# Performance work log

Hardware: AMD Instinct MI355X
Metric: run time of the kernel (lower is better)

## Reference

```python
import jax, jax.numpy as jnp
import numpy as np

B, T, H, CD, NC, S, D = 128, 256, 512, 128, 2048, 256, 9
EPS = 1e-5

def _lin(x, w, b):
    return x @ w.T + b

def _gru_cell(x, h, wih, whh, bih, bhh):
    gi = x @ wih.T + bih
    gh = h @ whh.T + bhh
    ir, iz, inn = jnp.split(gi, 3, axis=-1)
    hr, hz, hn = jnp.split(gh, 3, axis=-1)
    r = jax.nn.sigmoid(ir + hr)
    z = jax.nn.sigmoid(iz + hz)
    n = jnp.tanh(inn + r * hn)
    return (1.0 - z) * n + z * h

def _bn(x, g, b, m, v):
    # eval-mode BatchNorm1d over channel dim of [B,C,W]
    return (x - m[:, None]) * (g * jax.lax.rsqrt(v + EPS))[:, None] + b[:, None]

def _conv(x, w, b, stride, pad):
    y = jax.lax.conv_general_dilated(x, w, (stride,), [(pad, pad)], dimension_numbers=('NCW', 'OIW', 'NCW'))
    return y + b[:, None]

def _convT(x, w, b, stride, pad, out_pad):
    # torch ConvTranspose1d with weight [I,O,k] == dilated conv with flipped, transposed kernel
    k = w.shape[-1]
    w2 = jnp.flip(w, -1).transpose(1, 0, 2)  # [O,I,k]
    y = jax.lax.conv_general_dilated(x, w2, (1,), [(k - 1 - pad, k - 1 - pad + out_pad)], lhs_dilation=(stride,), dimension_numbers=('NCW', 'OIW', 'NCW'))
    return y + b[:, None]

def _gru_seq(x, h0, wih, whh, bih, bhh, reverse=False):
    def step(h, xt):
        hn = _gru_cell(xt, h, wih, whh, bih, bhh)
        return hn, hn
    _, ys = jax.lax.scan(step, h0, jnp.swapaxes(x, 0, 1), reverse=reverse)
    return jnp.swapaxes(ys, 0, 1)

def _forward(note, skel, skel_encoded, ehw, ehb, ifw, ifb, gfwih, gfwhh, gfbih, gfbhh, gbwih, gbwhh, gbbih, gbbhh, bn0g, bn0b, bn0m, bn0v, c1w, c1b, bn1g, bn1b, bn1m, bn1v, c2w, c2b, bn2g, bn2b, bn2m, bn2v, c3w, c3b, embed, ct1w, ct1b, dbn1g, dbn1b, dbn1m, dbn1v, ct2w, ct2b, dbn2g, dbn2b, dbn2m, dbn2v, dhw, dhb, g1wih, g1whh, g1bih, g1bhh, g2wih, g2whh, g2bih, g2bhh, nfw, nfb, samp_rand):
    sg = jax.lax.stop_gradient
    # ---- encoder ----
    hid = _lin(skel_encoded, ehw, ehb)                         # [B,H] shared init for both GRU dirs
    x = _lin(note, ifw, ifb)                                   # [B,T,H]
    fwd = _gru_seq(x, hid, gfwih, gfwhh, gfbih, gfbhh)
    bwd = _gru_seq(x, hid, gbwih, gbwhh, gbbih, gbbhh, reverse=True)
    out = jnp.concatenate([fwd, bwd], axis=-1).transpose(0, 2, 1)  # [B,2H,T]
    out = _bn(out, bn0g, bn0b, bn0m, bn0v)
    out = jax.nn.leaky_relu(_bn(_conv(out, c1w, c1b, 2, 1), bn1g, bn1b, bn1m, bn1v), 0.2)
    out = jax.nn.leaky_relu(_bn(_conv(out, c2w, c2b, 2, 1), bn2g, bn2b, bn2m, bn2v), 0.2)
    z = _conv(out, c3w, c3b, 1, 0)                             # [B,CD,T//4]
    # ---- vector quantizer (eval: no EMA update) ----
    zt = z.transpose(0, 2, 1)                                  # [B,T//4,CD]
    flat = zt.reshape(-1, CD)
    dist = (flat * flat).sum(1, keepdims=True) - 2.0 * flat @ embed.T + (embed * embed).sum(1)
    idx = jnp.argmin(dist, axis=1)                             # [B*T//4]
    quant = embed[idx].reshape(zt.shape)
    codebook_loss = jnp.mean((sg(quant) - zt) ** 2)
    cmt_loss = jnp.mean((quant - sg(zt)) ** 2)
    loss = codebook_loss + 0.2 * cmt_loss
    quant_st = zt + sg(quant - zt)                             # straight-through
    qz = quant_st.transpose(0, 2, 1)                           # [B,CD,T//4]
    avg_probs = jnp.zeros((NC,), zt.dtype).at[idx].add(1.0) / idx.shape[0]
    perplexity = jnp.exp(-jnp.sum(avg_probs * jnp.log(avg_probs + 1e-10)))
    enc_idx = idx.reshape(B, -1, 1)
    # ---- decoder ----
    d = jax.nn.leaky_relu(_bn(_convT(qz, ct1w, ct1b, 2, 0, 1), dbn1g, dbn1b, dbn1m, dbn1v), 0.2)
    d = jax.nn.leaky_relu(_bn(_convT(d, ct2w, ct2b, 2, 0, 0), dbn2g, dbn2b, dbn2m, dbn2v), 0.2)
    dec_in = d.transpose(0, 2, 1)                              # [B,T+8,H//2]
    h1 = _lin(skel_encoded, dhw, dhb)
    out0 = jnp.zeros((B, D), zt.dtype)
    cat0 = jnp.concatenate([out0, dec_in[:, 0], skel[:, 0]], axis=-1)
    h1 = _gru_cell(cat0, h1, g1wih, g1whh, g1bih, g1bhh)
    h2 = _gru_cell(h1, h1, g2wih, g2whh, g2bih, g2bhh)         # hx[1] init = hx[0] at i==0
    logit0 = _lin(h2, nfw, nfb)
    fb0 = (jax.nn.sigmoid(logit0) - samp_rand[0] > 0).astype(zt.dtype)  # eval-mode bernoulli sample
    def step(carry, xs):
        fb, h1, h2 = carry
        inp_i, skel_i, rand_i = xs
        h1 = _gru_cell(jnp.concatenate([fb, inp_i, skel_i], axis=-1), h1, g1wih, g1whh, g1bih, g1bhh)
        h2 = _gru_cell(h1, h2, g2wih, g2whh, g2bih, g2bhh)
        logits = _lin(h2, nfw, nfb)
        fb = (jax.nn.sigmoid(logits) - rand_i > 0).astype(logits.dtype)
        return (fb, h1, h2), logits
    xs = (jnp.swapaxes(dec_in[:, 1:T], 0, 1), jnp.swapaxes(skel[:, 1:T], 0, 1), samp_rand[1:T])
    _, logits_rest = jax.lax.scan(step, (fb0, h1, h2), xs)
    note_recon = jnp.swapaxes(jnp.concatenate([logit0[None], logits_rest], axis=0), 0, 1)  # [B,T,D]
    return note_recon, qz, loss, cmt_loss, enc_idx, perplexity

def setup_inputs():
    key = jax.random.key(0)
    ks = iter(jax.random.split(key, 96))
    nrm = lambda *s: jax.random.normal(next(ks), s, jnp.float32) * 0.05
    uni = lambda *s: jax.random.uniform(next(ks), s, jnp.float32)
    def bnp(c):
        g = 1.0 + 0.1 * jax.random.normal(next(ks), (c,), jnp.float32)
        b = nrm(c)
        m = nrm(c) * 2.0
        v = jax.random.uniform(next(ks), (c,), jnp.float32, 0.5, 1.5)
        return g, b, m, v
    inp = {}
    inp['note'] = uni(B, T, D)
    inp['skel'] = uni(B, T, D)
    inp['skel_encoded'] = jax.random.normal(next(ks), (B, S), jnp.float32)
    inp['ehw'] = nrm(H, S); inp['ehb'] = nrm(H)
    inp['ifw'] = nrm(H, D); inp['ifb'] = nrm(H)
    inp['gfwih'] = nrm(3 * H, H); inp['gfwhh'] = nrm(3 * H, H); inp['gfbih'] = nrm(3 * H); inp['gfbhh'] = nrm(3 * H)
    inp['gbwih'] = nrm(3 * H, H); inp['gbwhh'] = nrm(3 * H, H); inp['gbbih'] = nrm(3 * H); inp['gbbhh'] = nrm(3 * H)
    inp['bn0g'], inp['bn0b'], inp['bn0m'], inp['bn0v'] = bnp(2 * H)
    inp['c1w'] = nrm(H, 2 * H, 4); inp['c1b'] = nrm(H)
    inp['bn1g'], inp['bn1b'], inp['bn1m'], inp['bn1v'] = bnp(H)
    inp['c2w'] = nrm(H, H, 4); inp['c2b'] = nrm(H)
    inp['bn2g'], inp['bn2b'], inp['bn2m'], inp['bn2v'] = bnp(H)
    inp['c3w'] = nrm(CD, H, 1); inp['c3b'] = nrm(CD)
    inp['embed'] = jax.random.normal(next(ks), (NC, CD), jnp.float32)  # torch normal_() init, std 1
    inp['ct1w'] = nrm(CD, H, 4); inp['ct1b'] = nrm(H)
    inp['dbn1g'], inp['dbn1b'], inp['dbn1m'], inp['dbn1v'] = bnp(H)
    inp['ct2w'] = nrm(H, H // 2, 4); inp['ct2b'] = nrm(H // 2)
    inp['dbn2g'], inp['dbn2b'], inp['dbn2m'], inp['dbn2v'] = bnp(H // 2)
    inp['dhw'] = nrm(H, S); inp['dhb'] = nrm(H)
    inp['g1wih'] = nrm(3 * H, H // 2 + 2 * D); inp['g1whh'] = nrm(3 * H, H); inp['g1bih'] = nrm(3 * H); inp['g1bhh'] = nrm(3 * H)
    inp['g2wih'] = nrm(3 * H, H); inp['g2whh'] = nrm(3 * H, H); inp['g2bih'] = nrm(3 * H); inp['g2bhh'] = nrm(3 * H)
    inp['nfw'] = nrm(D, H); inp['nfb'] = nrm(D)
    inp['samp_rand'] = uni(T, B, D)  # pre-drawn noise for eval-mode bernoulli sampling
    inp['training'] = 0
    inp['teacher_forcing_ratio'] = 0
    return inp

def reference(note, skel, skel_encoded, ehw, ehb, ifw, ifb, gfwih, gfwhh, gfbih, gfbhh, gbwih, gbwhh, gbbih, gbbhh, bn0g, bn0b, bn0m, bn0v, c1w, c1b, bn1g, bn1b, bn1m, bn1v, c2w, c2b, bn2g, bn2b, bn2m, bn2v, c3w, c3b, embed, ct1w, ct1b, dbn1g, dbn1b, dbn1m, dbn1v, ct2w, ct2b, dbn2g, dbn2b, dbn2m, dbn2v, dhw, dhb, g1wih, g1whh, g1bih, g1bhh, g2wih, g2whh, g2bih, g2bhh, nfw, nfb, samp_rand, training, teacher_forcing_ratio):
    # eval path: training flag unused (dropout off, BN running stats, no EMA, always sample)
    return _forward(note, skel, skel_encoded, ehw, ehb, ifw, ifb, gfwih, gfwhh, gfbih, gfbhh, gbwih, gbwhh, gbbih, gbbhh, bn0g, bn0b, bn0m, bn0v, c1w, c1b, bn1g, bn1b, bn1m, bn1v, c2w, c2b, bn2g, bn2b, bn2m, bn2v, c3w, c3b, embed, ct1w, ct1b, dbn1g, dbn1b, dbn1m, dbn1v, ct2w, ct2b, dbn2g, dbn2b, dbn2m, dbn2v, dhw, dhb, g1wih, g1whh, g1bih, g1bhh, g2wih, g2whh, g2bih, g2bhh, nfw, nfb, samp_rand)
```

## Files before the change

### kernel.cpp

```cpp
#include <hip/hip_runtime.h>
#include <math.h>


#define DI __device__ __forceinline__

#define O_HF   ((size_t)0)
#define O_HB   ((size_t)131072)
#define O_H1   ((size_t)262144)
#define O_H2   ((size_t)393216)
#define O_WEFF ((size_t)524288)
#define O_BEFF ((size_t)551936)
#define O_BNS  ((size_t)555008)
#define O_ESQ  ((size_t)560640)
#define O_HIST ((size_t)562688)
#define O_RED  ((size_t)564736)
#define O_LOG  ((size_t)564752)
#define O_IDX  ((size_t)567056)
#define O_ZT   ((size_t)575248)
#define O_QT   ((size_t)1623824)
#define O_C2   ((size_t)2672400)
#define O_C1   ((size_t)6866704)
#define O_WT1  ((size_t)15255312)
#define O_WT2  ((size_t)17352464)
#define O_WT3  ((size_t)18401040)
#define O_WTD1 ((size_t)18466576)
#define O_WTD2 ((size_t)18728720)
#define O_YS   ((size_t)19253008)
#define O_D1   O_YS
#define O_DEC  (O_YS + (size_t)8388608)

#define ESOFF ((size_t)2672400)
#define DSOFF ((size_t)36030224)

#define BN0S 0
#define BN0T 1024
#define BN1S 2048
#define BN1T 2560
#define BN2S 3072
#define BN2T 3584
#define DB1S 4096
#define DB1T 4608
#define DB2S 5120
#define DB2T 5376

#define OUT_NR   0
#define OUT_QZ   294912
#define OUT_LOSS 1343488
#define OUT_CMT  1343489
#define OUT_IDX  1343490
#define OUT_PERP 1351682

DI float sigm(float x){ return 1.0f/(1.0f + expf(-x)); }

typedef __attribute__((ext_vector_type(8))) short s8v;
typedef __attribute__((ext_vector_type(4))) float f32x4;

DI f32x4 MF(s8v a, s8v b, f32x4 c){
  return __builtin_amdgcn_mfma_f32_16x16x32_bf16(a, b, c, 0, 0, 0);
}
DI s8v LD8(const unsigned short* p){ return *(const s8v*)p; }

DI void split3(float x, unsigned short& o0, unsigned short& o1, unsigned short& o2){
  unsigned u0 = __float_as_uint(x);
  unsigned h0 = (u0 + 0x7fffu + ((u0>>16)&1u)) >> 16;
  float x1 = x - __uint_as_float(h0<<16);
  unsigned u1 = __float_as_uint(x1);
  unsigned h1 = (u1 + 0x7fffu + ((u1>>16)&1u)) >> 16;
  float x2 = x1 - __uint_as_float(h1<<16);
  unsigned u2 = __float_as_uint(x2);
  unsigned h2 = (u2 + 0x7fffu + ((u2>>16)&1u)) >> 16;
  o0 = (unsigned short)h0; o1 = (unsigned short)h1; o2 = (unsigned short)h2;
}

#define MF8(A0,A1,A2,Q0,Q1,Q2,C0,C1) \
  C0 = MF(A0,Q0,C0); C1 = MF(A0,Q1,C1); \
  C0 = MF(A1,Q1,C0); C1 = MF(A1,Q0,C1); \
  C0 = MF(A0,Q2,C0); C1 = MF(A2,Q0,C1); \
  C0 = MF(A2,Q1,C0); C1 = MF(A1,Q2,C1);

#define FMA44 \
  acc[0][0] += a4.x*b4.x; acc[0][1] += a4.x*b4.y; acc[0][2] += a4.x*b4.z; acc[0][3] += a4.x*b4.w; \
  acc[1][0] += a4.y*b4.x; acc[1][1] += a4.y*b4.y; acc[1][2] += a4.y*b4.z; acc[1][3] += a4.y*b4.w; \
  acc[2][0] += a4.z*b4.x; acc[2][1] += a4.z*b4.y; acc[2][2] += a4.z*b4.z; acc[2][3] += a4.z*b4.w; \
  acc[3][0] += a4.w*b4.x; acc[3][1] += a4.w*b4.y; acc[3][2] += a4.w*b4.z; acc[3][3] += a4.w*b4.w;

__global__ void trans_kern(const float* __restrict__ c1w, const float* __restrict__ c2w,
                           const float* __restrict__ c3w, const float* __restrict__ ct1w,
                           const float* __restrict__ ct2w, float* __restrict__ ws){
  const int A1 = 2097152, A2 = 3145728, A3 = 3211264, A4 = 3473408, A5 = 3997696;
  for (int i = blockIdx.x*256 + threadIdx.x; i < A5; i += gridDim.x*256){
    if (i < A1){
      int j = i; int oc = j & 511; int t = j >> 9; int ic = t & 1023; int k = t >> 10;
      ws[O_WT1 + j] = c1w[((size_t)oc*1024 + ic)*4 + k];
    } else if (i < A2){
      int j = i - A1; int oc = j & 511; int t = j >> 9; int ic = t & 511; int k = t >> 9;
      ws[O_WT2 + j] = c2w[((size_t)oc*512 + ic)*4 + k];
    } else if (i < A3){
      int j = i - A2; int oc = j & 127; int ic = j >> 7;
      ws[O_WT3 + j] = c3w[(size_t)oc*512 + ic];
    } else if (i < A4){
      int j = i - A3; int oc = j & 511; int t = j >> 9; int ic = t & 127; int k = t >> 7;
      ws[O_WTD1 + j] = ct1w[((size_t)ic*512 + oc)*4 + k];
    } else {
      int j = i - A4; int oc = j & 255; int t = j >> 8; int ic = t & 511; int k = t >> 9;
      ws[O_WTD2 + j] = ct2w[((size_t)ic*256 + oc)*4 + k];
    }
  }
}

__global__ void bn_kern(const float* g0,const float* b0,const float* m0,const float* v0,
                        const float* g1,const float* b1,const float* m1,const float* v1,
                        const float* g2,const float* b2,const float* m2,const float* v2,
                        const float* gd1,const float* bd1,const float* md1,const float* vd1,
                        const float* gd2,const float* bd2,const float* md2,const float* vd2,
                        float* __restrict__ bns){
  int i = blockIdx.x*256 + threadIdx.x;
  if (i >= 2816) return;
  const float *g,*b,*m,*v; int c, so, to;
  if (i < 1024){ g=g0;b=b0;m=m0;v=v0;c=i;so=BN0S;to=BN0T; }
  else if (i < 1536){ g=g1;b=b1;m=m1;v=v1;c=i-1024;so=BN1S;to=BN1T; }
  else if (i < 2048){ g=g2;b=b2;m=m2;v=v2;c=i-1536;so=BN2S;to=BN2T; }
  else if (i < 2560){ g=gd1;b=bd1;m=md1;v=vd1;c=i-2048;so=DB1S;to=DB1T; }
  else              { g=gd2;b=bd2;m=md2;v=vd2;c=i-2560;so=DB2S;to=DB2T; }
  float s = g[c]*rsqrtf(v[c] + 1e-5f);
  bns[so + c] = s;
  bns[to + c] = b[c] - m[c]*s;
}

__global__ __launch_bounds__(256) void init_kern(const float* __restrict__ se,
    const float* __restrict__ ehw, const float* __restrict__ ehb,
    const float* __restrict__ dhw, const float* __restrict__ dhb, float* __restrict__ ws){
  int idx = blockIdx.x*256 + threadIdx.x;
  int n = idx & 1023, b = idx >> 10;
  const float* w; float bias;
  if (n < 512){ w = ehw + (size_t)n*256; bias = ehb[n]; }
  else        { w = dhw + (size_t)(n-512)*256; bias = dhb[n-512]; }
  const float* sp = se + (size_t)b*256;
  float acc = bias;
  for (int k = 0; k < 256; ++k) acc += sp[k]*w[k];
  if (n < 512){
    ws[O_HF + 65536 + b*512 + n] = acc;
    ws[O_HB + 65536 + b*512 + n] = acc;
    unsigned short s0,s1,s2; split3(acc, s0,s1,s2);
    unsigned short* esh = (unsigned short*)(ws + ESOFF) + 4718592;
    int off = 196608 + b*512 + n;
    esh[off] = s0; esh[off+65536] = s1; esh[off+131072] = s2;
    esh[393216+off] = s0; esh[393216+off+65536] = s1; esh[393216+off+131072] = s2;
  } else {
    ws[O_H1 + 65536 + b*512 + (n-512)] = acc;
  }
}

__global__ __launch_bounds__(256) void weff_kern(const float* __restrict__ gfwih,
    const float* __restrict__ gfbih, const float* __restrict__ gbwih, const float* __restrict__ gbbih,
    const float* __restrict__ ifw, const float* __restrict__ ifb, float* __restrict__ ws){
  int idx = blockIdx.x*256 + threadIdx.x;
  if (idx >= 30720) return;
  int dir = idx / 15360; int r = idx - dir*15360;
  int j3 = r / 10; int d = r - j3*10;
  const float* wih = dir ? gbwih : gfwih;
  float acc = 0.f;
  if (d < 9){
    for (int k = 0; k < 512; ++k) acc += wih[(size_t)j3*512 + k]*ifw[k*9 + d];
    ws[O_WEFF + dir*13824 + j3*9 + d] = acc;
  } else {
    for (int k = 0; k < 512; ++k) acc += wih[(size_t)j3*512 + k]*ifb[k];
    acc += (dir ? gbbih : gfbih)[j3];
    ws[O_BEFF + dir*1536 + j3] = acc;
  }
}

__global__ __launch_bounds__(256) void esq_kern(const float* __restrict__ embed, float* __restrict__ ws){
  int e = blockIdx.x*256 + threadIdx.x;
  float acc = 0.f;
  for (int c = 0; c < 128; ++c){ float t = embed[(size_t)e*128 + c]; acc += t*t; }
  ws[O_ESQ + e] = acc;
  if (blockIdx.x == 0){
    for (int i = threadIdx.x; i < 2048; i += 256) ws[O_HIST + i] = 0.f;
    if (threadIdx.x < 16) ws[O_RED + threadIdx.x] = 0.f;
  }
}

__global__ void split_w_kern(const float* __restrict__ gfwhh,
    const float* __restrict__ gbwhh, float* __restrict__ ws){
  unsigned short* es = (unsigned short*)(ws + ESOFF);
  for (int i = blockIdx.x*256 + threadIdx.x; i < 1572864; i += gridDim.x*256){
    int half = i >= 786432;
    int idx = i - (half ? 786432 : 0);
    float x = half ? gbwhh[idx] : gfwhh[idx];
    unsigned short s0,s1,s2; split3(x,s0,s1,s2);
    unsigned short* d = es + (half ? 2359296 : 0);
    d[idx] = s0; d[idx+786432] = s1; d[idx+1572864] = s2;
  }
}

__global__ void split_w2_kern(const float* __restrict__ g1wih, const float* __restrict__ g1whh,
    const float* __restrict__ g2wih, const float* __restrict__ g2whh, float* __restrict__ ws){
  unsigned short* dsb = (unsigned short*)(ws + DSOFF);
  const int total = 393216 + 3*786432 + 65536;
  for (int i = blockIdx.x*256 + threadIdx.x; i < total; i += gridDim.x*256){
    float x; unsigned short* d; int off, stride;
    if (i < 393216){
      int row = i>>8, k = i&255;
      x = g1wih[(size_t)row*274 + 9 + k]; d = dsb; off = i; stride = 393216;
    } else if (i < 1179648){
      int idx = i-393216; x = g1whh[idx]; d = dsb + 1179648; off = idx; stride = 786432;
    } else if (i < 1966080){
      int idx = i-1179648; x = g2wih[idx]; d = dsb + 3538944; off = idx; stride = 786432;
    } else if (i < 2752512){
      int idx = i-1966080; x = g2whh[idx]; d = dsb + 5898240; off = idx; stride = 786432;
    } else {
      int idx = i-2752512; x = ws[O_H1 + 65536 + idx];
      d = dsb + 8257536 + 196608; off = idx; stride = 65536;
    }
    unsigned short s0,s1,s2; split3(x,s0,s1,s2);
    d[off] = s0; d[off+stride] = s1; d[off+2*stride] = s2;
  }
}

__global__ void split_dec_kern(float* __restrict__ ws){
  unsigned short* decs = (unsigned short*)(ws + ESOFF);
  const float* dec = ws + O_DEC;
  for (int i = blockIdx.x*256 + threadIdx.x; i < 8388608; i += gridDim.x*256){
    unsigned short s0,s1,s2; split3(dec[i],s0,s1,s2);
    decs[i] = s0; decs[i+8388608] = s1; decs[i+16777216] = s2;
  }
}

__global__ __launch_bounds__(256) void enc_step_mfma(
    float* __restrict__ ws, const float* __restrict__ note,
    const float* __restrict__ gfbhh, const float* __restrict__ gbbhh, int step){
  int bi = blockIdx.x;
  int dir = bi>>7, bt = (bi>>5)&3, jt = bi&31;
  int b0 = bt*32, j0 = jt*16;
  int tid = threadIdx.x, w = tid>>6, l = tid&63;
  int m = w&1, kh = w>>1;
  int pb = (step+1)&1, cb = step&1;
  float* hprev = ws + (dir? O_HB : O_HF) + (size_t)pb*65536;
  float* hnext = ws + (dir? O_HB : O_HF) + (size_t)cb*65536;
  unsigned short* esh = (unsigned short*)(ws + ESOFF) + 4718592 + dir*393216;
  const unsigned short* hsp = esh + pb*196608;
  unsigned short* hsn = esh + cb*196608;
  const unsigned short* wsp = (const unsigned short*)(ws + ESOFF) + dir*2359296;
  const float* weff = ws + O_WEFF + dir*13824;
  const float* beff = ws + O_BEFF + dir*1536;
  const float* bhh = dir? gbbhh : gfbhh;
  const float* bns = ws + O_BNS;
  float* ys = ws + O_YS;

  const unsigned short* ab = hsp + (b0 + m*16 + (l&15))*512 + kh*256 + ((l>>4)<<3);
  const unsigned short* bb = wsp + (j0 + (l&15))*512 + kh*256 + ((l>>4)<<3);
  f32x4 z4 = {0.f,0.f,0.f,0.f};
  f32x4 acc[3][2] = {{z4,z4},{z4,z4},{z4,z4}};
  #pragma unroll
  for (int kt = 0; kt < 8; ++kt){
    s8v a0 = LD8(ab + kt*32);
    s8v a1 = LD8(ab + 65536 + kt*32);
    s8v a2 = LD8(ab + 131072 + kt*32);
    #pragma unroll
    for (int g = 0; g < 3; ++g){
      const unsigned short* bp = bb + g*262144 + kt*32;
      s8v q0 = LD8(bp);
      s8v q1 = LD8(bp + 786432);
      s8v q2 = LD8(bp + 1572864);
      MF8(a0,a1,a2, q0,q1,q2, acc[g][0], acc[g][1])
    }
  }
  __shared__ float red[3072];
  #pragma unroll
  for (int g = 0; g < 3; ++g){
    f32x4 s = acc[g][0] + acc[g][1];
    #pragma unroll
    for (int i = 0; i < 4; ++i) red[((w*3+g)<<8) + (i<<6) + l] = s[i];
  }
  __syncthreads();
  int t = dir ? 255-step : step;
  #pragma unroll
  for (int ii = 0; ii < 2; ++ii){
    int i = kh*2 + ii;
    int b = b0 + m*16 + ((l>>4)<<2) + i;
    int j = j0 + (l&15);
    float Y[3];
    #pragma unroll
    for (int g = 0; g < 3; ++g)
      Y[g] = red[((m*3+g)<<8)+(i<<6)+l] + red[((m*3+g+6)<<8)+(i<<6)+l];
    const float* nt = note + ((size_t)b*256 + t)*9;
    float gi[3];
    #pragma unroll
    for (int g = 0; g < 3; ++g){
      const float* wr = weff + (size_t)(g*512+j)*9;
      float a = beff[g*512+j];
      #pragma unroll
      for (int d = 0; d < 9; ++d) a += nt[d]*wr[d];
      gi[g] = a;
    }
    float hpv = hprev[(size_t)b*512 + j];
    float r = sigm(gi[0] + Y[0] + bhh[j]);
    float zz = sigm(gi[1] + Y[1] + bhh[512+j]);
    float nn = tanhf(gi[2] + r*(Y[2] + bhh[1024+j]));
    float h = (1.f - zz)*nn + zz*hpv;
    hnext[(size_t)b*512 + j] = h;
    unsigned short s0,s1,s2; split3(h, s0,s1,s2);
    int off = b*512 + j;
    hsn[off] = s0; hsn[off+65536] = s1; hsn[off+131072] = s2;
    int c = dir*512 + j;
    ys[((size_t)b*256 + t)*1024 + c] = h*bns[BN0S + c] + bns[BN0T + c];
  }
}

__global__ __launch_bounds__(256) void dec_k1_mfma(
    float* __restrict__ ws, const float* __restrict__ skel, const float* __restrict__ sr,
    const float* __restrict__ w1ih, const float* __restrict__ b1ih,
    const float* __restrict__ b1hh, const float* __restrict__ nfb,
    float* __restrict__ dout, int step){
  int bi = blockIdx.x;
  int bt = bi>>5, jt = bi&31;
  int b0 = bt*16, j0 = jt*16;
  int tid = threadIdx.x, w = tid>>6, l = tid&63;
  int kh = w;
  int pb = (step+1)&1, cb = step&1;
  const float* h1p = ws + O_H1 + (size_t)pb*65536;
  float* h1n = ws + O_H1 + (size_t)cb*65536;
  const float* logp = ws + O_LOG + (size_t)pb*1152;
  float* logc = ws + O_LOG + (size_t)cb*1152;
  unsigned short* dsb = (unsigned short*)(ws + DSOFF);
  const unsigned short* h1sp = dsb + 8257536 + pb*196608;
  unsigned short* h1sn = dsb + 8257536 + cb*196608;
  const unsigned short* decs = (const unsigned short*)(ws + ESOFF);
  const unsigned short* w1d = dsb;
  const unsigned short* w1h = dsb + 1179648;

  __shared__ float fbs[144], ssh[144];
  __shared__ float red[6144];
  if (tid < 144){
    int bb = tid/9, d = tid - bb*9; int b = b0 + bb;
    float fv = 0.f;
    if (step > 0){
      float lg = logp[b*9 + d];
      fv = (1.f/(1.f + expf(-lg)) - sr[(size_t)(step-1)*1152 + b*9 + d]) > 0.f ? 1.f : 0.f;
    }
    fbs[tid] = fv;
    ssh[tid] = skel[((size_t)b*256 + step)*9 + d];
  }
  if (bi == 0){
    for (int idx = tid; idx < 1152; idx += 256){
      logc[idx] = nfb[idx % 9];
      if (step > 0) dout[OUT_NR + (size_t)(idx/9)*2304 + (step-1)*9 + (idx%9)] = logp[idx];
    }
  }
  f32x4 z4 = {0.f,0.f,0.f,0.f};
  f32x4 gia[3][2] = {{z4,z4},{z4,z4},{z4,z4}};
  f32x4 gha[3][2] = {{z4,z4},{z4,z4},{z4,z4}};
  {
    const unsigned short* ab = decs + (b0 + (l&15))*65536 + step*256 + kh*64 + ((l>>4)<<3);
    const unsigned short* bb = w1d + (j0 + (l&15))*256 + kh*64 + ((l>>4)<<3);
    #pragma unroll
    for (int kt = 0; kt < 2; ++kt){
      s8v a0 = LD8(ab + kt*32);
      s8v a1 = LD8(ab + 8388608 + kt*32);
      s8v a2 = LD8(ab + 16777216 + kt*32);
      #pragma unroll
      for (int g = 0; g < 3; ++g){
        const unsigned short* bp = bb + g*131072 + kt*32;
        s8v q0 = LD8(bp);
        s8v q1 = LD8(bp + 393216);
        s8v q2 = LD8(bp + 786432);
        MF8(a0,a1,a2, q0,q1,q2, gia[g][0], gia[g][1])
      }
    }
  }
  {
    const unsigned short* ab = h1sp + (b0 + (l&15))*512 + kh*128 + ((l>>4)<<3);
    const unsigned short* bb = w1h + (j0 + (l&15))*512 + kh*128 + ((l>>4)<<3);
    #pragma unroll
    for (int kt = 0; kt < 4; ++kt){
      s8v a0 = LD8(ab + kt*32);
      s8v a1 = LD8(ab + 65536 + kt*32);
      s8v a2 = LD8(ab + 131072 + kt*32);
      #pragma unroll
      for (int g = 0; g < 3; ++g){
        const unsigned short* bp = bb + g*262144 + kt*32;
        s8v q0 = LD8(bp);
        s8v q1 = LD8(bp + 786432);
        s8v q2 = LD8(bp + 1572864);
        MF8(a0,a1,a2, q0,q1,q2, gha[g][0], gha[g][1])
      }
    }
  }
  #pragma unroll
  for (int g = 0; g < 3; ++g){
    f32x4 s = gia[g][0] + gia[g][1];
    f32x4 t = gha[g][0] + gha[g][1];
    #pragma unroll
    for (int i = 0; i < 4; ++i){
      red[((w*6+g)<<8) + (i<<6) + l] = s[i];
      red[((w*6+g+3)<<8) + (i<<6) + l] = t[i];
    }
  }
  __syncthreads();
  int i = w;
  int b = b0 + ((l>>4)<<2) + i;
  int j = j0 + (l&15);
  float GI[3], GH[3];
  #pragma unroll
  for (int pg = 0; pg < 3; ++pg){
    float a = 0.f, c = 0.f;
    #pragma unroll
    for (int ww = 0; ww < 4; ++ww){
      a += red[((ww*6+pg)<<8)+(i<<6)+l];
      c += red[((ww*6+pg+3)<<8)+(i<<6)+l];
    }
    GI[pg] = a; GH[pg] = c;
  }
  int bb = b - b0;
  #pragma unroll
  for (int g = 0; g < 3; ++g){
    const float* wr = w1ih + (size_t)(g*512+j)*274;
    float a = GI[g] + b1ih[g*512+j];
    #pragma unroll
    for (int d = 0; d < 9; ++d) a += fbs[bb*9+d]*wr[d] + ssh[bb*9+d]*wr[265+d];
    GI[g] = a;
  }
  float hpv = h1p[(size_t)b*512 + j];
  float r = sigm(GI[0] + GH[0] + b1hh[j]);
  float zz = sigm(GI[1] + GH[1] + b1hh[512+j]);
  float nn = tanhf(GI[2] + r*(GH[2] + b1hh[1024+j]));
  float h = (1.f-zz)*nn + zz*hpv;
  h1n[(size_t)b*512 + j] = h;
  unsigned short s0,s1,s2; split3(h,s0,s1,s2);
  int off = b*512 + j;
  h1sn[off] = s0; h1sn[off+65536] = s1; h1sn[off+131072] = s2;
}

__global__ __launch_bounds__(256) void dec_k2_mfma(
    float* __restrict__ ws, const float* __restrict__ b2ih, const float* __restrict__ b2hh,
    const float* __restrict__ nfw, int step){
  int bi = blockIdx.x;
  int bt = bi>>5, jt = bi&31;
  int b0 = bt*16, j0 = jt*16;
  int tid = threadIdx.x, w = tid>>6, l = tid&63;
  int kh = w;
  int pb = (step+1)&1, cb = step&1;
  const float* h1n = ws + O_H1 + (size_t)cb*65536;
  const float* h2p = (step==0) ? h1n : ws + O_H2 + (size_t)pb*65536;
  float* h2n = ws + O_H2 + (size_t)cb*65536;
  float* logc = ws + O_LOG + (size_t)cb*1152;
  unsigned short* dsb = (unsigned short*)(ws + DSOFF);
  const unsigned short* h1sn = dsb + 8257536 + cb*196608;
  const unsigned short* h2sp = (step==0) ? h1sn : dsb + 8650752 + pb*196608;
  unsigned short* h2sn = dsb + 8650752 + cb*196608;
  const unsigned short* w2i = dsb + 3538944;
  const unsigned short* w2h = dsb + 5898240;

  __shared__ float red[6144];
  __shared__ float hsm[256];
  f32x4 z4 = {0.f,0.f,0.f,0.f};
  f32x4 gia[3][2] = {{z4,z4},{z4,z4},{z4,z4}};
  f32x4 gha[3][2] = {{z4,z4},{z4,z4},{z4,z4}};
  {
    const unsigned short* ab = h1sn + (b0 + (l&15))*512 + kh*128 + ((l>>4)<<3);
    const unsigned short* bb = w2i + (j0 + (l&15))*512 + kh*128 + ((l>>4)<<3);
    #pragma unroll
    for (int kt = 0; kt < 4; ++kt){
      s8v a0 = LD8(ab + kt*32);
      s8v a1 = LD8(ab + 65536 + kt*32);
      s8v a2 = LD8(ab + 131072 + kt*32);
      #pragma unroll
      for (int g = 0; g < 3; ++g){
        const unsigned short* bp = bb + g*262144 + kt*32;
        s8v q0 = LD8(bp);
        s8v q1 = LD8(bp + 786432);
        s8v q2 = LD8(bp + 1572864);
        MF8(a0,a1,a2, q0,q1,q2, gia[g][0], gia[g][1])
      }
    }
  }
  {
    const unsigned short* ab = h2sp + (b0 + (l&15))*512 + kh*128 + ((l>>4)<<3);
    const unsigned short* bb = w2h + (j0 + (l&15))*512 + kh*128 + ((l>>4)<<3);
    #pragma unroll
    for (int kt = 0; kt < 4; ++kt){
      s8v a0 = LD8(ab + kt*32);
      s8v a1 = LD8(ab + 65536 + kt*32);
      s8v a2 = LD8(ab + 131072 + kt*32);
      #pragma unroll
      for (int g = 0; g < 3; ++g){
        const unsigned short* bp = bb + g*262144 + kt*32;
        s8v q0 = LD8(bp);
        s8v q1 = LD8(bp + 786432);
        s8v q2 = LD8(bp + 1572864);
        MF8(a0,a1,a2, q0,q1,q2, gha[g][0], gha[g][1])
      }
    }
  }
  #pragma unroll
  for (int g = 0; g < 3; ++g){
    f32x4 s = gia[g][0] + gia[g][1];
    f32x4 t = gha[g][0] + gha[g][1];
    #pragma unroll
    for (int i = 0; i < 4; ++i){
      red[((w*6+g)<<8) + (i<<6) + l] = s[i];
      red[((w*6+g+3)<<8) + (i<<6) + l] = t[i];
    }
  }
  __syncthreads();
  int i = w;
  int b = b0 + ((l>>4)<<2) + i;
  int j = j0 + (l&15);
  float GI[3], GH[3];
  #pragma unroll
  for (int pg = 0; pg < 3; ++pg){
    float a = 0.f, c = 0.f;
    #pragma unroll
    for (int ww = 0; ww < 4; ++ww){
      a += red[((ww*6+pg)<<8)+(i<<6)+l];
      c += red[((ww*6+pg+3)<<8)+(i<<6)+l];
    }
    GI[pg] = a; GH[pg] = c;
  }
  float hpv = h2p[(size_t)b*512 + j];
  float r = sigm(GI[0] + b2ih[j] + GH[0] + b2hh[j]);
  float zz = sigm(GI[1] + b2ih[512+j] + GH[1] + b2hh[512+j]);
  float nn = tanhf(GI[2] + b2ih[1024+j] + r*(GH[2] + b2hh[1024+j]));
  float h = (1.f-zz)*nn + zz*hpv;
  h2n[(size_t)b*512 + j] = h;
  unsigned short s0,s1,s2; split3(h,s0,s1,s2);
  int off = b*512 + j;
  h2sn[off] = s0; h2sn[off+65536] = s1; h2sn[off+131072] = s2;
  hsm[(b-b0)*16 + (j-j0)] = h;
  __syncthreads();
  if (tid < 144){
    int bq = tid/9, d = tid - bq*9;
    float v = 0.f;
    #pragma unroll
    for (int jl = 0; jl < 16; ++jl) v += hsm[bq*16+jl]*nfw[(size_t)d*512 + j0 + jl];
    atomicAdd(&logc[(b0+bq)*9 + d], v);
  }
}

__global__ __launch_bounds__(256) void conv1_kern(const float* __restrict__ ysb,
    const float* __restrict__ wt, const float* __restrict__ cb,
    const float* __restrict__ bns, float* __restrict__ outp){
  int gm = blockIdx.x, gn = blockIdx.y;
  int b = gm >> 1, ot0 = (gm & 1) << 6, oc0 = gn << 6;
  int tid = threadIdx.x, tx = tid & 15, ty = tid >> 4;
  __shared__ __align__(16) float As[32*68];
  __shared__ __align__(16) float Bs[32*68];
  float acc[4][4] = {};
  for (int k = 0; k < 4; ++k){
    for (int ic0 = 0; ic0 < 1024; ic0 += 32){
      #pragma unroll
      for (int rr = 0; rr < 8; ++rr){
        int e = rr*256 + tid; int m = e >> 5, ic = e & 31;
        int tin = ((ot0 + m) << 1) + k - 1;
        float v = 0.f;
        if ((unsigned)tin < 256u) v = ysb[((size_t)b*256 + tin)*1024 + ic0 + ic];
        As[ic*68 + m] = v;
      }
      #pragma unroll
      for (int rr = 0; rr < 8; ++rr){
        int e = rr*256 + tid; int oc = e & 63, ic = e >> 6;
        Bs[ic*68 + oc] = wt[((size_t)k*1024 + ic0 + ic)*512 + oc0 + oc];
      }
      __syncthreads();
      #pragma unroll
      for (int kk = 0; kk < 32; ++kk){
        float4 a4 = *(const float4*)&As[kk*68 + ty*4];
        float4 b4 = *(const float4*)&Bs[kk*68 + tx*4];
        FMA44
      }
      __syncthreads();
    }
  }
  #pragma unroll
  for (int i = 0; i < 4; ++i){
    int ot = ot0 + ty*4 + i;
    #pragma unroll
    for (int jj = 0; jj < 4; ++jj){
      int oc = oc0 + tx*4 + jj;
      float v = acc[i][jj] + cb[oc];
      v = v*bns[BN1S + oc] + bns[BN1T + oc];
      v = v > 0.f ? v : 0.2f*v;
      outp[((size_t)b*128 + ot)*512 + oc] = v;
    }
  }
}

__global__ __launch_bounds__(256) void conv2_kern(const float* __restrict__ c1o,
    const float* __restrict__ wt, const float* __restrict__ cb,
    const float* __restrict__ bns, float* __restrict__ outp){
  int b = blockIdx.x, oc0 = blockIdx.y << 6;
  int tid = threadIdx.x, tx = tid & 15, ty = tid >> 4;
  __shared__ __align__(16) float As[32*68];
  __shared__ __align__(16) float Bs[32*68];
  float acc[4][4] = {};
  for (int k = 0; k < 4; ++k){
    for (int ic0 = 0; ic0 < 512; ic0 += 32){
      #pragma unroll
      for (int rr = 0; rr < 8; ++rr){
        int e = rr*256 + tid; int m = e >> 5, ic = e & 31;
        int tin = (m << 1) + k - 1;
        float v = 0.f;
        if ((unsigned)tin < 128u) v = c1o[((size_t)b*128 + tin)*512 + ic0 + ic];
        As[ic*68 + m] = v;
      }
      #pragma unroll
      for (int rr = 0; rr < 8; ++rr){
        int e = rr*256 + tid; int oc = e & 63, ic = e >> 6;
        Bs[ic*68 + oc] = wt[((size_t)k*512 + ic0 + ic)*512 + oc0 + oc];
      }
      __syncthreads();
      #pragma unroll
      for (int kk = 0; kk < 32; ++kk){
        float4 a4 = *(const float4*)&As[kk*68 + ty*4];
        float4 b4 = *(const float4*)&Bs[kk*68 + tx*4];
        FMA44
      }
      __syncthreads();
    }
  }
  #pragma unroll
  for (int i = 0; i < 4; ++i){
    int ot = ty*4 + i;
    #pragma unroll
    for (int jj = 0; jj < 4; ++jj){
      int oc = oc0 + tx*4 + jj;
      float v = acc[i][jj] + cb[oc];
      v = v*bns[BN2S + oc] + bns[BN2T + oc];
      v = v > 0.f ? v : 0.2f*v;
      outp[((size_t)b*64 + ot)*512 + oc] = v;
    }
  }
}

__global__ __launch_bounds__(256) void conv3_kern(const float* __restrict__ c2o,
    const float* __restrict__ wt, const float* __restrict__ cb, float* __restrict__ zt){
  int row0 = blockIdx.x << 6, oc0 = blockIdx.y << 6;
  int tid = threadIdx.x, tx = tid & 15, ty = tid >> 4;
  __shared__ __align__(16) float As[32*68];
  __shared__ __align__(16) float Bs[32*68];
  float acc[4][4] = {};
  for (int ic0 = 0; ic0 < 512; ic0 += 32){
    #pragma unroll
    for (int rr = 0; rr < 8; ++rr){
      int e = rr*256 + tid; int m = e >> 5, ic = e & 31;
      As[ic*68 + m] = c2o[((size_t)(row0 + m))*512 + ic0 + ic];
    }
    #pragma unroll
    for (int rr = 0; rr < 8; ++rr){
      int e = rr*256 + tid; int oc = e & 63, ic = e >> 6;
      Bs[ic*68 + oc] = wt[(size_t)(ic0 + ic)*128 + oc0 + oc];
    }
    __syncthreads();
    #pragma unroll
    for (int kk = 0; kk < 32; ++kk){
      float4 a4 = *(const float4*)&As[kk*68 + ty*4];
      float4 b4 = *(const float4*)&Bs[kk*68 + tx*4];
      FMA44
    }
    __syncthreads();
  }
  #pragma unroll
  for (int i = 0; i < 4; ++i){
    int row = row0 + ty*4 + i;
    #pragma unroll
    for (int jj = 0; jj < 4; ++jj){
      int oc = oc0 + tx*4 + jj;
      zt[(size_t)row*128 + oc] = acc[i][jj] + cb[oc];
    }
  }
}

__global__ __launch_bounds__(256) void vq_kern(const float* __restrict__ zt,
    const float* __restrict__ esq, const float* __restrict__ embed,
    int* __restrict__ idxp, float* __restrict__ hist, float* __restrict__ dout){
  int r0 = blockIdx.x * 8;
  int tid = threadIdx.x;
  int r = tid >> 5, el = tid & 31;
  __shared__ __align__(16) float zsh[1024];
  __shared__ __align__(16) float esh[4096];
  __shared__ float rv[256]; __shared__ int ri[256];
  for (int idx = tid; idx < 1024; idx += 256) zsh[idx] = zt[(size_t)r0*128 + idx];
  float minv = 3.4e38f; int mini = 0;
  for (int e0 = 0; e0 < 2048; e0 += 32){
    for (int idx = tid; idx < 4096; idx += 256){
      int ee = idx >> 7, c = idx & 127;
      esh[ee*128 + ((((c >> 2) ^ (ee & 31)) & 31) << 2) + (c & 3)] = embed[(size_t)(e0 + ee)*128 + c];
    }
    __syncthreads();
    float dot = 0.f;
    #pragma unroll
    for (int c0 = 0; c0 < 128; c0 += 4){
      float4 zq = *(const float4*)&zsh[r*128 + c0];
      float4 e4 = *(const float4*)&esh[el*128 + ((((c0 >> 2) ^ (el & 31)) & 31) << 2)];
      dot += zq.x*e4.x + zq.y*e4.y + zq.z*e4.z + zq.w*e4.w;
    }
    float d = esq[e0 + el] - 2.f*dot;
    if (d < minv){ minv = d; mini = e0 + el; }
    __syncthreads();
  }
  rv[tid] = minv; ri[tid] = mini;
  __syncthreads();
  for (int off = 16; off > 0; off >>= 1){
    if (el < off){
      float ov = rv[tid + off]; int oi = ri[tid + off];
      if (ov < rv[tid] || (ov == rv[tid] && oi < ri[tid])){ rv[tid] = ov; ri[tid] = oi; }
    }
    __syncthreads();
  }
  if (el == 0){
    int row = r0 + r; int best = ri[tid];
    idxp[row] = best;
    dout[OUT_IDX + row] = (float)best;
    atomicAdd(&hist[best], 1.f);
  }
}

__global__ __launch_bounds__(256) void quant_kern(const float* __restrict__ zt,
    const int* __restrict__ idxp, const float* __restrict__ embed,
    float* __restrict__ qt, float* __restrict__ redp, float* __restrict__ dout){
  float local = 0.f;
  #pragma unroll
  for (int rr = 0; rr < 4; ++rr){
    int i = blockIdx.x*1024 + rr*256 + threadIdx.x;
    int c = i & 127, p = (i >> 7) & 63, b = i >> 13;
    int e = idxp[b*64 + p];
    float q = embed[(size_t)e*128 + c];
    float d = q - zt[i];
    local += d*d;
    qt[i] = q;
    dout[OUT_QZ + ((size_t)b*128 + c)*64 + p] = q;
  }
  __shared__ float red[256];
  red[threadIdx.x] = local; __syncthreads();
  for (int off = 128; off; off >>= 1){
    if (threadIdx.x < off) red[threadIdx.x] += red[threadIdx.x + off];
    __syncthreads();
  }
  if (threadIdx.x == 0) atomicAdd(redp, red[0]);
}

__global__ __launch_bounds__(256) void perp_kern(const float* __restrict__ hist,
    const float* __restrict__ redp, float* __restrict__ dout){
  __shared__ float red[256];
  float local = 0.f;
  for (int i = threadIdx.x; i < 2048; i += 256){
    float p = hist[i] * (1.f/8192.f);
    local += p * logf(p + 1e-10f);
  }
  red[threadIdx.x] = local; __syncthreads();
  for (int off = 128; off; off >>= 1){
    if (threadIdx.x < off) red[threadIdx.x] += red[threadIdx.x + off];
    __syncthreads();
  }
  if (threadIdx.x == 0){
    float mse = redp[0] * (1.f/1048576.f);
    dout[OUT_LOSS] = 1.2f*mse;
    dout[OUT_CMT]  = mse;
    dout[OUT_PERP] = expf(-red[0]);
  }
}

__global__ __launch_bounds__(256) void convt1_kern(const float* __restrict__ qt,
    const float* __restrict__ wt, const float* __restrict__ cb,
    const float* __restrict__ bns, float* __restrict__ d1){
  int gm = blockIdx.x;
  int b = gm >> 1, op0 = (gm & 1) << 6, oc0 = blockIdx.y << 6;
  int tid = threadIdx.x, tx = tid & 15, ty = tid >> 4;
  __shared__ __align__(16) float As[32*68];
  __shared__ __align__(16) float Bs[32*68];
  float acc[4][4] = {};
  for (int k = 0; k < 4; ++k){
    for (int ic0 = 0; ic0 < 128; ic0 += 32){
      #pragma unroll
      for (int rr = 0; rr < 8; ++rr){
        int e = rr*256 + tid; int m = e >> 5, ic = e & 31;
        int op = op0 + m;
        float v = 0.f;
        if (op >= k && (((op - k) & 1) == 0)){
          int ip = (op - k) >> 1;
          v = qt[((size_t)b*64 + ip)*128 + ic0 + ic];
        }
        As[ic*68 + m] = v;
      }
      #pragma unroll
      for (int rr = 0; rr < 8; ++rr){
        int e = rr*256 + tid; int oc = e & 63, ic = e >> 6;
        Bs[ic*68 + oc] = wt[((size_t)k*128 + ic0 + ic)*512 + oc0 + oc];
      }
      __syncthreads();
      #pragma unroll
      for (int kk = 0; kk < 32; ++kk){
        float4 a4 = *(const float4*)&As[kk*68 + ty*4];
        float4 b4 = *(const float4*)&Bs[kk*68 + tx*4];
        FMA44
      }
      __syncthreads();
    }
  }
  #pragma unroll
  for (int i = 0; i < 4; ++i){
    int op = op0 + ty*4 + i;
    #pragma unroll
    for (int jj = 0; jj < 4; ++jj){
      int oc = oc0 + tx*4 + jj;
      float v = acc[i][jj] + cb[oc];
      v = v*bns[DB1S + oc] + bns[DB1T + oc];
      v = v > 0.f ? v : 0.2f*v;
      d1[((size_t)b*128 + op)*512 + oc] = v;
    }
  }
}

__global__ __launch_bounds__(256) void convt2_kern(const float* __restrict__ d1,
    const float* __restrict__ wt, const float* __restrict__ cb,
    const float* __restrict__ bns, float* __restrict__ dec){
  int gm = blockIdx.x;
  int b = gm >> 2, op0 = (gm & 3) << 6, oc0 = blockIdx.y << 6;
  int tid = threadIdx.x, tx = tid & 15, ty = tid >> 4;
  __shared__ __align__(16) float As[32*68];
  __shared__ __align__(16) float Bs[32*68];
  float acc[4][4] = {};
  for (int k = 0; k < 4; ++k){
    for (int ic0 = 0; ic0 < 512; ic0 += 32){
      #pragma unroll
      for (int rr = 0; rr < 8; ++rr){
        int e = rr*256 + tid; int m = e >> 5, ic = e & 31;
        int op = op0 + m;
        float v = 0.f;
        if (op >= k && (((op - k) & 1) == 0)){
          int ip = (op - k) >> 1;
          v = d1[((size_t)b*128 + ip)*512 + ic0 + ic];
        }
        As[ic*68 + m] = v;
      }
      #pragma unroll
      for (int rr = 0; rr < 8; ++rr){
        int e = rr*256 + tid; int oc = e & 63, ic = e >> 6;
        Bs[ic*68 + oc] = wt[((size_t)k*512 + ic0 + ic)*256 + oc0 + oc];
      }
      __syncthreads();
      #pragma unroll
      for (int kk = 0; kk < 32; ++kk){
        float4 a4 = *(const float4*)&As[kk*68 + ty*4];
        float4 b4 = *(const float4*)&Bs[kk*68 + tx*4];
        FMA44
      }
      __syncthreads();
    }
  }
  #pragma unroll
  for (int i = 0; i < 4; ++i){
    int op = op0 + ty*4 + i;
    #pragma unroll
    for (int jj = 0; jj < 4; ++jj){
      int oc = oc0 + tx*4 + jj;
      float v = acc[i][jj] + cb[oc];
      v = v*bns[DB2S + oc] + bns[DB2T + oc];
      v = v > 0.f ? v : 0.2f*v;
      dec[((size_t)b*256 + op)*256 + oc] = v;
    }
  }
}

__global__ void copylast_kern(const float* __restrict__ logit1, float* __restrict__ dout){
  int idx = blockIdx.x*256 + threadIdx.x;
  if (idx < 1152) dout[OUT_NR + (size_t)(idx/9)*2304 + 255*9 + (idx % 9)] = logit1[idx];
}

extern "C" void kernel_launch(void* const* d_in, const int* in_sizes, int n_in,
                              void* d_out, int out_size, void* d_ws, size_t ws_size,
                              hipStream_t stream){
  (void)in_sizes; (void)n_in; (void)out_size; (void)ws_size;
  const float* note  = (const float*)d_in[0];
  const float* skel  = (const float*)d_in[1];
  const float* se    = (const float*)d_in[2];
  const float* ehw   = (const float*)d_in[3];
  const float* ehb   = (const float*)d_in[4];
  const float* ifw   = (const float*)d_in[5];
  const float* ifb   = (const float*)d_in[6];
  const float* gfwih = (const float*)d_in[7];
  const float* gfwhh = (const float*)d_in[8];
  const float* gfbih = (const float*)d_in[9];
  const float* gfbhh = (const float*)d_in[10];
  const float* gbwih = (const float*)d_in[11];
  const float* gbwhh = (const float*)d_in[12];
  const float* gbbih = (const float*)d_in[13];
  const float* gbbhh = (const float*)d_in[14];
  const float* bn0g  = (const float*)d_in[15];
  const float* bn0b  = (const float*)d_in[16];
  const float* bn0m  = (const float*)d_in[17];
  const float* bn0v  = (const float*)d_in[18];
  const float* c1w   = (const float*)d_in[19];
  const float* c1b   = (const float*)d_in[20];
  const float* bn1g  = (const float*)d_in[21];
  const float* bn1b  = (const float*)d_in[22];
  const float* bn1m  = (const float*)d_in[23];
  const float* bn1v  = (const float*)d_in[24];
  const float* c2w   = (const float*)d_in[25];
  const float* c2b   = (const float*)d_in[26];
  const float* bn2g  = (const float*)d_in[27];
  const float* bn2b  = (const float*)d_in[28];
  const float* bn2m  = (const float*)d_in[29];
  const float* bn2v  = (const float*)d_in[30];
  const float* c3w   = (const float*)d_in[31];
  const float* c3b   = (const float*)d_in[32];
  const float* embed = (const float*)d_in[33];
  const float* ct1w  = (const float*)d_in[34];
  const float* ct1b  = (const float*)d_in[35];
  const float* dbn1g = (const float*)d_in[36];
  const float* dbn1b = (const float*)d_in[37];
  const float* dbn1m = (const float*)d_in[38];
  const float* dbn1v = (const float*)d_in[39];
  const float* ct2w  = (const float*)d_in[40];
  const float* ct2b  = (const float*)d_in[41];
  const float* dbn2g = (const float*)d_in[42];
  const float* dbn2b = (const float*)d_in[43];
  const float* dbn2m = (const float*)d_in[44];
  const float* dbn2v = (const float*)d_in[45];
  const float* dhw   = (const float*)d_in[46];
  const float* dhb   = (const float*)d_in[47];
  const float* g1wih = (const float*)d_in[48];
  const float* g1whh = (const float*)d_in[49];
  const float* g1bih = (const float*)d_in[50];
  const float* g1bhh = (const float*)d_in[51];
  const float* g2wih = (const float*)d_in[52];
  const float* g2whh = (const float*)d_in[53];
  const float* g2bih = (const float*)d_in[54];
  const float* g2bhh = (const float*)d_in[55];
  const float* nfw   = (const float*)d_in[56];
  const float* nfb   = (const float*)d_in[57];
  const float* sr    = (const float*)d_in[58];

  float* ws  = (float*)d_ws;
  float* out = (float*)d_out;
  float* ysp  = ws + O_YS;
  float* bnsp = ws + O_BNS;

  trans_kern<<<dim3(2048), dim3(256), 0, stream>>>(c1w, c2w, c3w, ct1w, ct2w, ws);
  bn_kern<<<dim3(11), dim3(256), 0, stream>>>(bn0g,bn0b,bn0m,bn0v, bn1g,bn1b,bn1m,bn1v,
                                              bn2g,bn2b,bn2m,bn2v, dbn1g,dbn1b,dbn1m,dbn1v,
                                              dbn2g,dbn2b,dbn2m,dbn2v, bnsp);
  init_kern<<<dim3(512), dim3(256), 0, stream>>>(se, ehw, ehb, dhw, dhb, ws);
  weff_kern<<<dim3(120), dim3(256), 0, stream>>>(gfwih, gfbih, gbwih, gbbih, ifw, ifb, ws);
  esq_kern<<<dim3(8), dim3(256), 0, stream>>>(embed, ws);
  split_w_kern<<<dim3(1024), dim3(256), 0, stream>>>(gfwhh, gbwhh, ws);

  for (int s = 0; s < 256; ++s){
    enc_step_mfma<<<dim3(256), dim3(256), 0, stream>>>(ws, note, gfbhh, gbbhh, s);
  }

  conv1_kern<<<dim3(256, 8), dim3(256), 0, stream>>>(ysp, ws + O_WT1, c1b, bnsp, ws + O_C1);
  split_w2_kern<<<dim3(2048), dim3(256), 0, stream>>>(g1wih, g1whh, g2wih, g2whh, ws);
  conv2_kern<<<dim3(128, 8), dim3(256), 0, stream>>>(ws + O_C1, ws + O_WT2, c2b, bnsp, ws + O_C2);
  conv3_kern<<<dim3(128, 2), dim3(256), 0, stream>>>(ws + O_C2, ws + O_WT3, c3b, ws + O_ZT);

  vq_kern<<<dim3(1024), dim3(256), 0, stream>>>(ws + O_ZT, ws + O_ESQ, embed,
      (int*)(ws + O_IDX), ws + O_HIST, out);
  quant_kern<<<dim3(1024), dim3(256), 0, stream>>>(ws + O_ZT, (const int*)(ws + O_IDX),
      embed, ws + O_QT, ws + O_RED, out);
  perp_kern<<<dim3(1), dim3(256), 0, stream>>>(ws + O_HIST, ws + O_RED, out);

  convt1_kern<<<dim3(256, 8), dim3(256), 0, stream>>>(ws + O_QT, ws + O_WTD1, ct1b, bnsp, ws + O_D1);
  convt2_kern<<<dim3(512, 4), dim3(256), 0, stream>>>(ws + O_D1, ws + O_WTD2, ct2b, bnsp, ws + O_DEC);
  split_dec_kern<<<dim3(2048), dim3(256), 0, stream>>>(ws);

  for (int i = 0; i < 256; ++i){
    dec_k1_mfma<<<dim3(256), dim3(256), 0, stream>>>(ws, skel, sr, g1wih, g1bih,
        g1bhh, nfb, out, i);
    dec_k2_mfma<<<dim3(256), dim3(256), 0, stream>>>(ws, g2bih, g2bhh, nfw, i);
  }
  copylast_kern<<<dim3(5), dim3(256), 0, stream>>>(ws + O_LOG + 1152, out);
}
```

Before: 14.94 ms.

## Replace per-step GRU launches with persistent cooperative kernels using team barriers

The 256 per-timestep encoder launches and 512 decoder launches are replaced by two persistent cooperative kernels. Each loops over time steps internally and synchronises only the group of blocks that share a batch tile, using an atomic-counter spin barrier. Per-thread constants (input-projection weights, biases, BN scale) are hoisted into registers. The atomicAdd logit accumulation becomes per-column-tile partial sums reduced on the next step. This removes launch overhead and full-grid serialization, but adds spin-wait cost and depends on all 256 blocks being co-resident.

```diff
diff --git a/kernel.cpp b/kernel.cpp
--- a/kernel.cpp
+++ b/kernel.cpp
@@ -29,6 +29,9 @@
 #define O_D1   O_YS
 #define O_DEC  (O_YS + (size_t)8388608)
 
+#define O_CTR  O_C1
+#define O_PLOG O_ZT
+
 #define ESOFF ((size_t)2672400)
 #define DSOFF ((size_t)36030224)
 
@@ -83,6 +86,18 @@
   acc[1][0] += a4.y*b4.x; acc[1][1] += a4.y*b4.y; acc[1][2] += a4.y*b4.z; acc[1][3] += a4.y*b4.w; \
   acc[2][0] += a4.z*b4.x; acc[2][1] += a4.z*b4.y; acc[2][2] += a4.z*b4.z; acc[2][3] += a4.z*b4.w; \
   acc[3][0] += a4.w*b4.x; acc[3][1] += a4.w*b4.y; acc[3][2] += a4.w*b4.z; acc[3][3] += a4.w*b4.w;
+
+DI void team_barrier(unsigned* c, unsigned target){
+  __syncthreads();
+  if (threadIdx.x == 0){
+    __threadfence();
+    atomicAdd(c, 1u);
+    while (__hip_atomic_load(c, __ATOMIC_RELAXED, __HIP_MEMORY_SCOPE_AGENT) < target)
+      __builtin_amdgcn_s_sleep(1);
+    __threadfence();
+  }
+  __syncthreads();
+}
 
 __global__ void trans_kern(const float* __restrict__ c1w, const float* __restrict__ c2w,
                            const float* __restrict__ c3w, const float* __restrict__ ct1w,
@@ -178,6 +193,7 @@
   if (blockIdx.x == 0){
     for (int i = threadIdx.x; i < 2048; i += 256) ws[O_HIST + i] = 0.f;
     if (threadIdx.x < 16) ws[O_RED + threadIdx.x] = 0.f;
+    if (threadIdx.x < 16) ((unsigned*)(ws + O_CTR))[threadIdx.x] = 0u;
   }
 }
 
@@ -221,320 +237,341 @@
 __global__ void split_dec_kern(float* __restrict__ ws){
   unsigned short* decs = (unsigned short*)(ws + ESOFF);
   const float* dec = ws + O_DEC;
+  if (blockIdx.x == 0 && threadIdx.x < 8)
+    ((unsigned*)(ws + O_CTR))[8 + threadIdx.x] = 0u;
   for (int i = blockIdx.x*256 + threadIdx.x; i < 8388608; i += gridDim.x*256){
     unsigned short s0,s1,s2; split3(dec[i],s0,s1,s2);
     decs[i] = s0; decs[i+8388608] = s1; decs[i+16777216] = s2;
   }
 }
 
-__global__ __launch_bounds__(256) void enc_step_mfma(
+__global__ __launch_bounds__(256) void enc_persist(
     float* __restrict__ ws, const float* __restrict__ note,
-    const float* __restrict__ gfbhh, const float* __restrict__ gbbhh, int step){
+    const float* __restrict__ gfbhh, const float* __restrict__ gbbhh){
   int bi = blockIdx.x;
   int dir = bi>>7, bt = (bi>>5)&3, jt = bi&31;
   int b0 = bt*32, j0 = jt*16;
   int tid = threadIdx.x, w = tid>>6, l = tid&63;
   int m = w&1, kh = w>>1;
-  int pb = (step+1)&1, cb = step&1;
-  float* hprev = ws + (dir? O_HB : O_HF) + (size_t)pb*65536;
-  float* hnext = ws + (dir? O_HB : O_HF) + (size_t)cb*65536;
+  unsigned* ctr = (unsigned*)(ws + O_CTR) + (dir*4 + bt);
+  float* hbase = ws + (dir? O_HB : O_HF);
   unsigned short* esh = (unsigned short*)(ws + ESOFF) + 4718592 + dir*393216;
-  const unsigned short* hsp = esh + pb*196608;
-  unsigned short* hsn = esh + cb*196608;
   const unsigned short* wsp = (const unsigned short*)(ws + ESOFF) + dir*2359296;
   const float* weff = ws + O_WEFF + dir*13824;
   const float* beff = ws + O_BEFF + dir*1536;
   const float* bhh = dir? gbbhh : gfbhh;
   const float* bns = ws + O_BNS;
   float* ys = ws + O_YS;
-
-  const unsigned short* ab = hsp + (b0 + m*16 + (l&15))*512 + kh*256 + ((l>>4)<<3);
-  const unsigned short* bb = wsp + (j0 + (l&15))*512 + kh*256 + ((l>>4)<<3);
-  f32x4 z4 = {0.f,0.f,0.f,0.f};
-  f32x4 acc[3][2] = {{z4,z4},{z4,z4},{z4,z4}};
-  #pragma unroll
-  for (int kt = 0; kt < 8; ++kt){
-    s8v a0 = LD8(ab + kt*32);
-    s8v a1 = LD8(ab + 65536 + kt*32);
-    s8v a2 = LD8(ab + 131072 + kt*32);
-    #pragma unroll
-    for (int g = 0; g < 3; ++g){
-      const unsigned short* bp = bb + g*262144 + kt*32;
-      s8v q0 = LD8(bp);
-      s8v q1 = LD8(bp + 786432);
-      s8v q2 = LD8(bp + 1572864);
-      MF8(a0,a1,a2, q0,q1,q2, acc[g][0], acc[g][1])
-    }
-  }
   __shared__ float red[3072];
+
+  int je = j0 + (l&15);
+  float wef[3][9], bef3[3], bhh3[3], bsc, bsh;
   #pragma unroll
   for (int g = 0; g < 3; ++g){
-    f32x4 s = acc[g][0] + acc[g][1];
-    #pragma unroll
-    for (int i = 0; i < 4; ++i) red[((w*3+g)<<8) + (i<<6) + l] = s[i];
-  }
-  __syncthreads();
-  int t = dir ? 255-step : step;
-  #pragma unroll
-  for (int ii = 0; ii < 2; ++ii){
-    int i = kh*2 + ii;
-    int b = b0 + m*16 + ((l>>4)<<2) + i;
-    int j = j0 + (l&15);
-    float Y[3];
-    #pragma unroll
-    for (int g = 0; g < 3; ++g)
-      Y[g] = red[((m*3+g)<<8)+(i<<6)+l] + red[((m*3+g+6)<<8)+(i<<6)+l];
-    const float* nt = note + ((size_t)b*256 + t)*9;
-    float gi[3];
+    bef3[g] = beff[g*512 + je];
+    #pragma unroll
+    for (int d = 0; d < 9; ++d) wef[g][d] = weff[(size_t)(g*512+je)*9 + d];
+    bhh3[g] = bhh[g*512 + je];
+  }
+  { int c = dir*512 + je; bsc = bns[BN0S + c]; bsh = bns[BN0T + c]; }
+
+  const unsigned short* bb = wsp + (size_t)(j0 + (l&15))*512 + kh*256 + ((l>>4)<<3);
+
+  #pragma unroll 1
+  for (int step = 0; step < 256; ++step){
+    int pb = (step+1)&1, cb = step&1;
+    const float* hprev = hbase + (size_t)pb*65536;
+    float*       hnext = hbase + (size_t)cb*65536;
+    const unsigned short* hsp = esh + pb*196608;
+    unsigned short*       hsn = esh + cb*196608;
+
+    const unsigned short* ab = hsp + (size_t)(b0 + m*16 + (l&15))*512 + kh*256 + ((l>>4)<<3);
+    f32x4 z4 = {0.f,0.f,0.f,0.f};
+    f32x4 acc[3][2] = {{z4,z4},{z4,z4},{z4,z4}};
+    #pragma unroll
+    for (int kt = 0; kt < 8; ++kt){
+      s8v a0 = LD8(ab + kt*32);
+      s8v a1 = LD8(ab + 65536 + kt*32);
+      s8v a2 = LD8(ab + 131072 + kt*32);
+      #pragma unroll
+      for (int g = 0; g < 3; ++g){
+        const unsigned short* bp = bb + g*262144 + kt*32;
+        s8v q0 = LD8(bp);
+        s8v q1 = LD8(bp + 786432);
+        s8v q2 = LD8(bp + 1572864);
+        MF8(a0,a1,a2, q0,q1,q2, acc[g][0], acc[g][1])
+      }
+    }
     #pragma unroll
     for (int g = 0; g < 3; ++g){
-      const float* wr = weff + (size_t)(g*512+j)*9;
-      float a = beff[g*512+j];
-      #pragma unroll
-      for (int d = 0; d < 9; ++d) a += nt[d]*wr[d];
-      gi[g] = a;
-    }
-    float hpv = hprev[(size_t)b*512 + j];
-    float r = sigm(gi[0] + Y[0] + bhh[j]);
-    float zz = sigm(gi[1] + Y[1] + bhh[512+j]);
-    float nn = tanhf(gi[2] + r*(Y[2] + bhh[1024+j]));
-    float h = (1.f - zz)*nn + zz*hpv;
-    hnext[(size_t)b*512 + j] = h;
-    unsigned short s0,s1,s2; split3(h, s0,s1,s2);
-    int off = b*512 + j;
-    hsn[off] = s0; hsn[off+65536] = s1; hsn[off+131072] = s2;
-    int c = dir*512 + j;
-    ys[((size_t)b*256 + t)*1024 + c] = h*bns[BN0S + c] + bns[BN0T + c];
-  }
-}
-
-__global__ __launch_bounds__(256) void dec_k1_mfma(
+      f32x4 s = acc[g][0] + acc[g][1];
+      #pragma unroll
+      for (int i = 0; i < 4; ++i) red[((w*3+g)<<8) + (i<<6) + l] = s[i];
+    }
+    __syncthreads();
+    int t = dir ? 255-step : step;
+    #pragma unroll
+    for (int ii = 0; ii < 2; ++ii){
+      int i = kh*2 + ii;
+      int b = b0 + m*16 + ((l>>4)<<2) + i;
+      float Y[3];
+      #pragma unroll
+      for (int g = 0; g < 3; ++g)
+        Y[g] = red[((m*3+g)<<8)+(i<<6)+l] + red[((m*3+g+6)<<8)+(i<<6)+l];
+      const float* nt = note + ((size_t)b*256 + t)*9;
+      float gi[3];
+      #pragma unroll
+      for (int g = 0; g < 3; ++g){
+        float a = bef3[g];
+        #pragma unroll
+        for (int d = 0; d < 9; ++d) a += nt[d]*wef[g][d];
+        gi[g] = a;
+      }
+      float hpv = hprev[(size_t)b*512 + je];
+      float r = sigm(gi[0] + Y[0] + bhh3[0]);
+      float zz = sigm(gi[1] + Y[1] + bhh3[1]);
+      float nn = tanhf(gi[2] + r*(Y[2] + bhh3[2]));
+      float h = (1.f - zz)*nn + zz*hpv;
+      hnext[(size_t)b*512 + je] = h;
+      unsigned short s0,s1,s2; split3(h, s0,s1,s2);
+      int off = b*512 + je;
+      hsn[off] = s0; hsn[off+65536] = s1; hsn[off+131072] = s2;
+      int c = dir*512 + je;
+      ys[((size_t)b*256 + t)*1024 + c] = h*bsc + bsh;
+    }
+    team_barrier(ctr, 32u*(step+1));
+  }
+}
+
+__global__ __launch_bounds__(256) void dec_persist(
     float* __restrict__ ws, const float* __restrict__ skel, const float* __restrict__ sr,
     const float* __restrict__ w1ih, const float* __restrict__ b1ih,
     const float* __restrict__ b1hh, const float* __restrict__ nfb,
-    float* __restrict__ dout, int step){
+    const float* __restrict__ b2ih, const float* __restrict__ b2hh,
+    const float* __restrict__ nfw, float* __restrict__ dout){
   int bi = blockIdx.x;
   int bt = bi>>5, jt = bi&31;
   int b0 = bt*16, j0 = jt*16;
   int tid = threadIdx.x, w = tid>>6, l = tid&63;
   int kh = w;
-  int pb = (step+1)&1, cb = step&1;
-  const float* h1p = ws + O_H1 + (size_t)pb*65536;
-  float* h1n = ws + O_H1 + (size_t)cb*65536;
-  const float* logp = ws + O_LOG + (size_t)pb*1152;
-  float* logc = ws + O_LOG + (size_t)cb*1152;
+  unsigned* ctr = (unsigned*)(ws + O_CTR) + 8 + bt;
   unsigned short* dsb = (unsigned short*)(ws + DSOFF);
-  const unsigned short* h1sp = dsb + 8257536 + pb*196608;
-  unsigned short* h1sn = dsb + 8257536 + cb*196608;
   const unsigned short* decs = (const unsigned short*)(ws + ESOFF);
   const unsigned short* w1d = dsb;
   const unsigned short* w1h = dsb + 1179648;
-
+  const unsigned short* w2i = dsb + 3538944;
+  const unsigned short* w2h = dsb + 5898240;
+  float* plog = ws + O_PLOG;
   __shared__ float fbs[144], ssh[144];
   __shared__ float red[6144];
-  if (tid < 144){
+  __shared__ float hsm[256];
+
+  #pragma unroll 1
+  for (int step = 0; step < 256; ++step){
+    int pb = (step+1)&1, cb = step&1;
+    const float* h1p = ws + O_H1 + (size_t)pb*65536;
+    float*       h1n = ws + O_H1 + (size_t)cb*65536;
+    const unsigned short* h1sp = dsb + 8257536 + pb*196608;
+    unsigned short*       h1sn = dsb + 8257536 + cb*196608;
+
+    if (tid < 144){
+      int bb = tid/9, d = tid - bb*9; int b = b0 + bb;
+      float fv = 0.f;
+      if (step > 0){
+        float lg = nfb[d];
+        const float* pl = plog + (size_t)pb*36864 + b*9 + d;
+        #pragma unroll
+        for (int q = 0; q < 32; ++q) lg += pl[q*1152];
+        if (jt == 0) dout[OUT_NR + (size_t)b*2304 + (step-1)*9 + d] = lg;
+        fv = (sigm(lg) - sr[(size_t)(step-1)*1152 + b*9 + d]) > 0.f ? 1.f : 0.f;
+      }
+      fbs[tid] = fv;
+      ssh[tid] = skel[((size_t)b*256 + step)*9 + d];
+    }
+    f32x4 z4 = {0.f,0.f,0.f,0.f};
+    f32x4 gia[3][2] = {{z4,z4},{z4,z4},{z4,z4}};
+    f32x4 gha[3][2] = {{z4,z4},{z4,z4},{z4,z4}};
+    {
+      const unsigned short* ab = decs + (size_t)(b0 + (l&15))*65536 + step*256 + kh*64 + ((l>>4)<<3);
+      const unsigned short* bbp = w1d + (size_t)(j0 + (l&15))*256 + kh*64 + ((l>>4)<<3);
+      #pragma unroll
+      for (int kt = 0; kt < 2; ++kt){
+        s8v a0 = LD8(ab + kt*32);
+        s8v a1 = LD8(ab + 8388608 + kt*32);
+        s8v a2 = LD8(ab + 16777216 + kt*32);
+        #pragma unroll
+        for (int g = 0; g < 3; ++g){
+          const unsigned short* bp = bbp + g*131072 + kt*32;
+          s8v q0 = LD8(bp);
+          s8v q1 = LD8(bp + 393216);
+          s8v q2 = LD8(bp + 786432);
+          MF8(a0,a1,a2, q0,q1,q2, gia[g][0], gia[g][1])
+        }
+      }
+    }
+    {
+      const unsigned short* ab = h1sp + (size_t)(b0 + (l&15))*512 + kh*128 + ((l>>4)<<3);
+      const unsigned short* bbp = w1h + (size_t)(j0 + (l&15))*512 + kh*128 + ((l>>4)<<3);
+      #pragma unroll
+      for (int kt = 0; kt < 4; ++kt){
+        s8v a0 = LD8(ab + kt*32);
+        s8v a1 = LD8(ab + 65536 + kt*32);
+        s8v a2 = LD8(ab + 131072 + kt*32);
+        #pragma unroll
+        for (int g = 0; g < 3; ++g){
+          const unsigned short* bp = bbp + g*262144 + kt*32;
+          s8v q0 = LD8(bp);
+          s8v q1 = LD8(bp + 786432);
+          s8v q2 = LD8(bp + 1572864);
+          MF8(a0,a1,a2, q0,q1,q2, gha[g][0], gha[g][1])
+        }
+      }
+    }
+    #pragma unroll
+    for (int g = 0; g < 3; ++g){
+      f32x4 s = gia[g][0] + gia[g][1];
+      f32x4 t = gha[g][0] + gha[g][1];
+      #pragma unroll
+      for (int i = 0; i < 4; ++i){
+        red[((w*6+g)<<8) + (i<<6) + l] = s[i];
+        red[((w*6+g+3)<<8) + (i<<6) + l] = t[i];
+      }
+    }
+    __syncthreads();
+    {
+      int i = w;
+      int b = b0 + ((l>>4)<<2) + i;
+      int j = j0 + (l&15);
+      float GI[3], GH[3];
+      #pragma unroll
+      for (int pg = 0; pg < 3; ++pg){
+        float a = 0.f, c = 0.f;
+        #pragma unroll
+        for (int ww = 0; ww < 4; ++ww){
+          a += red[((ww*6+pg)<<8)+(i<<6)+l];
+          c += red[((ww*6+pg+3)<<8)+(i<<6)+l];
+        }
+        GI[pg] = a; GH[pg] = c;
+      }
+      int bb = b - b0;
+      #pragma unroll
+      for (int g = 0; g < 3; ++g){
+        const float* wr = w1ih + (size_t)(g*512+j)*274;
+        float a = GI[g] + b1ih[g*512+j];
+        #pragma unroll
+        for (int d = 0; d < 9; ++d) a += fbs[bb*9+d]*wr[d] + ssh[bb*9+d]*wr[265+d];
+        GI[g] = a;
+      }
+      float hpv = h1p[(size_t)b*512 + j];
+      float r = sigm(GI[0] + GH[0] + b1hh[j]);
+      float zz = sigm(GI[1] + GH[1] + b1hh[512+j]);
+      float nn = tanhf(GI[2] + r*(GH[2] + b1hh[1024+j]));
+      float h = (1.f-zz)*nn + zz*hpv;
+      h1n[(size_t)b*512 + j] = h;
+      unsigned short s0,s1,s2; split3(h,s0,s1,s2);
+      int off = b*512 + j;
+      h1sn[off] = s0; h1sn[off+65536] = s1; h1sn[off+131072] = s2;
+    }
+    team_barrier(ctr, 64u*step + 32u);
+
+    const float* h2p = (step==0) ? h1n : ws + O_H2 + (size_t)pb*65536;
+    float*       h2n = ws + O_H2 + (size_t)cb*65536;
+    const unsigned short* h2sp = (step==0) ? (const unsigned short*)h1sn
+                                           : dsb + 8650752 + pb*196608;
+    unsigned short* h2sn = dsb + 8650752 + cb*196608;
+
+    f32x4 kia[3][2] = {{z4,z4},{z4,z4},{z4,z4}};
+    f32x4 kha[3][2] = {{z4,z4},{z4,z4},{z4,z4}};
+    {
+      const unsigned short* ab = h1sn + (size_t)(b0 + (l&15))*512 + kh*128 + ((l>>4)<<3);
+      const unsigned short* bbp = w2i + (size_t)(j0 + (l&15))*512 + kh*128 + ((l>>4)<<3);
+      #pragma unroll
+      for (int kt = 0; kt < 4; ++kt){
+        s8v a0 = LD8(ab + kt*32);
+        s8v a1 = LD8(ab + 65536 + kt*32);
+        s8v a2 = LD8(ab + 131072 + kt*32);
+        #pragma unroll
+        for (int g = 0; g < 3; ++g){
+          const unsigned short* bp = bbp + g*262144 + kt*32;
+          s8v q0 = LD8(bp);
+          s8v q1 = LD8(bp + 786432);
+          s8v q2 = LD8(bp + 1572864);
+          MF8(a0,a1,a2, q0,q1,q2, kia[g][0], kia[g][1])
+        }
+      }
+    }
+    {
+      const unsigned short* ab = h2sp + (size_t)(b0 + (l&15))*512 + kh*128 + ((l>>4)<<3);
+      const unsigned short* bbp = w2h + (size_t)(j0 + (l&15))*512 + kh*128 + ((l>>4)<<3);
+      #pragma unroll
+      for (int kt = 0; kt < 4; ++kt){
+        s8v a0 = LD8(ab + kt*32);
+        s8v a1 = LD8(ab + 65536 + kt*32);
+        s8v a2 = LD8(ab + 131072 + kt*32);
+        #pragma unroll
+        for (int g = 0; g < 3; ++g){
+          const unsigned short* bp = bbp + g*262144 + kt*32;
+          s8v q0 = LD8(bp);
+          s8v q1 = LD8(bp + 786432);
+          s8v q2 = LD8(bp + 1572864);
+          MF8(a0,a1,a2, q0,q1,q2, kha[g][0], kha[g][1])
+        }
+      }
+    }
+    #pragma unroll
+    for (int g = 0; g < 3; ++g){
+      f32x4 s = kia[g][0] + kia[g][1];
+      f32x4 t = kha[g][0] + kha[g][1];
+      #pragma unroll
+      for (int i = 0; i < 4; ++i){
+        red[((w*6+g)<<8) + (i<<6) + l] = s[i];
+        red[((w*6+g+3)<<8) + (i<<6) + l] = t[i];
+      }
+    }
+    __syncthreads();
+    {
+      int i = w;
+      int b = b0 + ((l>>4)<<2) + i;
+      int j = j0 + (l&15);
+      float GI[3], GH[3];
+      #pragma unroll
+      for (int pg = 0; pg < 3; ++pg){
+        float a = 0.f, c = 0.f;
+        #pragma unroll
+        for (int ww = 0; ww < 4; ++ww){
+          a += red[((ww*6+pg)<<8)+(i<<6)+l];
+          c += red[((ww*6+pg+3)<<8)+(i<<6)+l];
+        }
+        GI[pg] = a; GH[pg] = c;
+      }
+      float hpv = h2p[(size_t)b*512 + j];
+      float r = sigm(GI[0] + b2ih[j] + GH[0] + b2hh[j]);
+      float zz = sigm(GI[1] + b2ih[512+j] + GH[1] + b2hh[512+j]);
+      float nn = tanhf(GI[2] + b2ih[1024+j] + r*(GH[2] + b2hh[1024+j]));
+      float h = (1.f-zz)*nn + zz*hpv;
+      h2n[(size_t)b*512 + j] = h;
+      unsigned short s0,s1,s2; split3(h,s0,s1,s2);
+      int off = b*512 + j;
+      h2sn[off] = s0; h2sn[off+65536] = s1; h2sn[off+131072] = s2;
+      hsm[(b-b0)*16 + (j-j0)] = h;
+    }
+    __syncthreads();
+    if (tid < 144){
+      int bq = tid/9, d = tid - bq*9;
+      float v = 0.f;
+      #pragma unroll
+      for (int jl = 0; jl < 16; ++jl) v += hsm[bq*16+jl]*nfw[(size_t)d*512 + j0 + jl];
+      plog[(size_t)cb*36864 + jt*1152 + (b0+bq)*9 + d] = v;
+    }
+    team_barrier(ctr, 64u*step + 64u);
+  }
+  if (jt == 0 && tid < 144){
     int bb = tid/9, d = tid - bb*9; int b = b0 + bb;
-    float fv = 0.f;
-    if (step > 0){
-      float lg = logp[b*9 + d];
-      fv = (1.f/(1.f + expf(-lg)) - sr[(size_t)(step-1)*1152 + b*9 + d]) > 0.f ? 1.f : 0.f;
-    }
-    fbs[tid] = fv;
-    ssh[tid] = skel[((size_t)b*256 + step)*9 + d];
-  }
-  if (bi == 0){
-    for (int idx = tid; idx < 1152; idx += 256){
-      logc[idx] = nfb[idx % 9];
-      if (step > 0) dout[OUT_NR + (size_t)(idx/9)*2304 + (step-1)*9 + (idx%9)] = logp[idx];
-    }
-  }
-  f32x4 z4 = {0.f,0.f,0.f,0.f};
-  f32x4 gia[3][2] = {{z4,z4},{z4,z4},{z4,z4}};
-  f32x4 gha[3][2] = {{z4,z4},{z4,z4},{z4,z4}};
-  {
-    const unsigned short* ab = decs + (b0 + (l&15))*65536 + step*256 + kh*64 + ((l>>4)<<3);
-    const unsigned short* bb = w1d + (j0 + (l&15))*256 + kh*64 + ((l>>4)<<3);
-    #pragma unroll
-    for (int kt = 0; kt < 2; ++kt){
-      s8v a0 = LD8(ab + kt*32);
-      s8v a1 = LD8(ab + 8388608 + kt*32);
-      s8v a2 = LD8(ab + 16777216 + kt*32);
-      #pragma unroll
-      for (int g = 0; g < 3; ++g){
-        const unsigned short* bp = bb + g*131072 + kt*32;
-        s8v q0 = LD8(bp);
-        s8v q1 = LD8(bp + 393216);
-        s8v q2 = LD8(bp + 786432);
-        MF8(a0,a1,a2, q0,q1,q2, gia[g][0], gia[g][1])
-      }
-    }
-  }
-  {
-    const unsigned short* ab = h1sp + (b0 + (l&15))*512 + kh*128 + ((l>>4)<<3);
-    const unsigned short* bb = w1h + (j0 + (l&15))*512 + kh*128 + ((l>>4)<<3);
-    #pragma unroll
-    for (int kt = 0; kt < 4; ++kt){
-      s8v a0 = LD8(ab + kt*32);
-      s8v a1 = LD8(ab + 65536 + kt*32);
-      s8v a2 = LD8(ab + 131072 + kt*32);
-      #pragma unroll
-      for (int g = 0; g < 3; ++g){
-        const unsigned short* bp = bb + g*262144 + kt*32;
-        s8v q0 = LD8(bp);
-        s8v q1 = LD8(bp + 786432);
-        s8v q2 = LD8(bp + 1572864);
-        MF8(a0,a1,a2, q0,q1,q2, gha[g][0], gha[g][1])
-      }
-    }
-  }
-  #pragma unroll
-  for (int g = 0; g < 3; ++g){
-    f32x4 s = gia[g][0] + gia[g][1];
-    f32x4 t = gha[g][0] + gha[g][1];
-    #pragma unroll
-    for (int i = 0; i < 4; ++i){
-      red[((w*6+g)<<8) + (i<<6) + l] = s[i];
-      red[((w*6+g+3)<<8) + (i<<6) + l] = t[i];
-    }
-  }
-  __syncthreads();
-  int i = w;
-  int b = b0 + ((l>>4)<<2) + i;
-  int j = j0 + (l&15);
-  float GI[3], GH[3];
-  #pragma unroll
-  for (int pg = 0; pg < 3; ++pg){
-    float a = 0.f, c = 0.f;
-    #pragma unroll
-    for (int ww = 0; ww < 4; ++ww){
-      a += red[((ww*6+pg)<<8)+(i<<6)+l];
-      c += red[((ww*6+pg+3)<<8)+(i<<6)+l];
-    }
-    GI[pg] = a; GH[pg] = c;
-  }
-  int bb = b - b0;
-  #pragma unroll
-  for (int g = 0; g < 3; ++g){
-    const float* wr = w1ih + (size_t)(g*512+j)*274;
-    float a = GI[g] + b1ih[g*512+j];
-    #pragma unroll
-    for (int d = 0; d < 9; ++d) a += fbs[bb*9+d]*wr[d] + ssh[bb*9+d]*wr[265+d];
-    GI[g] = a;
-  }
-  float hpv = h1p[(size_t)b*512 + j];
-  float r = sigm(GI[0] + GH[0] + b1hh[j]);
-  float zz = sigm(GI[1] + GH[1] + b1hh[512+j]);
-  float nn = tanhf(GI[2] + r*(GH[2] + b1hh[1024+j]));
-  float h = (1.f-zz)*nn + zz*hpv;
-  h1n[(size_t)b*512 + j] = h;
-  unsigned short s0,s1,s2; split3(h,s0,s1,s2);
-  int off = b*512 + j;
-  h1sn[off] = s0; h1sn[off+65536] = s1; h1sn[off+131072] = s2;
-}
-
-__global__ __launch_bounds__(256) void dec_k2_mfma(
-    float* __restrict__ ws, const float* __restrict__ b2ih, const float* __restrict__ b2hh,
-    const float* __restrict__ nfw, int step){
-  int bi = blockIdx.x;
-  int bt = bi>>5, jt = bi&31;
-  int b0 = bt*16, j0 = jt*16;
-  int tid = threadIdx.x, w = tid>>6, l = tid&63;
-  int kh = w;
-  int pb = (step+1)&1, cb = step&1;
-  const float* h1n = ws + O_H1 + (size_t)cb*65536;
-  const float* h2p = (step==0) ? h1n : ws + O_H2 + (size_t)pb*65536;
-  float* h2n = ws + O_H2 + (size_t)cb*65536;
-  float* logc = ws + O_LOG + (size_t)cb*1152;
-  unsigned short* dsb = (unsigned short*)(ws + DSOFF);
-  const unsigned short* h1sn = dsb + 8257536 + cb*196608;
-  const unsigned short* h2sp = (step==0) ? h1sn : dsb + 8650752 + pb*196608;
-  unsigned short* h2sn = dsb + 8650752 + cb*196608;
-  const unsigned short* w2i = dsb + 3538944;
-  const unsigned short* w2h = dsb + 5898240;
-
-  __shared__ float red[6144];
-  __shared__ float hsm[256];
-  f32x4 z4 = {0.f,0.f,0.f,0.f};
-  f32x4 gia[3][2] = {{z4,z4},{z4,z4},{z4,z4}};
-  f32x4 gha[3][2] = {{z4,z4},{z4,z4},{z4,z4}};
-  {
-    const unsigned short* ab = h1sn + (b0 + (l&15))*512 + kh*128 + ((l>>4)<<3);
-    const unsigned short* bb = w2i + (j0 + (l&15))*512 + kh*128 + ((l>>4)<<3);
-    #pragma unroll
-    for (int kt = 0; kt < 4; ++kt){
-      s8v a0 = LD8(ab + kt*32);
-      s8v a1 = LD8(ab + 65536 + kt*32);
-      s8v a2 = LD8(ab + 131072 + kt*32);
-      #pragma unroll
-      for (int g = 0; g < 3; ++g){
-        const unsigned short* bp = bb + g*262144 + kt*32;
-        s8v q0 = LD8(bp);
-        s8v q1 = LD8(bp + 786432);
-        s8v q2 = LD8(bp + 1572864);
-        MF8(a0,a1,a2, q0,q1,q2, gia[g][0], gia[g][1])
-      }
-    }
-  }
-  {
-    const unsigned short* ab = h2sp + (b0 + (l&15))*512 + kh*128 + ((l>>4)<<3);
-    const unsigned short* bb = w2h + (j0 + (l&15))*512 + kh*128 + ((l>>4)<<3);
-    #pragma unroll
-    for (int kt = 0; kt < 4; ++kt){
-      s8v a0 = LD8(ab + kt*32);
-      s8v a1 = LD8(ab + 65536 + kt*32);
-      s8v a2 = LD8(ab + 131072 + kt*32);
-      #pragma unroll
-      for (int g = 0; g < 3; ++g){
-        const unsigned short* bp = bb + g*262144 + kt*32;
-        s8v q0 = LD8(bp);
-        s8v q1 = LD8(bp + 786432);
-        s8v q2 = LD8(bp + 1572864);
-        MF8(a0,a1,a2, q0,q1,q2, gha[g][0], gha[g][1])
-      }
-    }
-  }
-  #pragma unroll
-  for (int g = 0; g < 3; ++g){
-    f32x4 s = gia[g][0] + gia[g][1];
-    f32x4 t = gha[g][0] + gha[g][1];
-    #pragma unroll
-    for (int i = 0; i < 4; ++i){
-      red[((w*6+g)<<8) + (i<<6) + l] = s[i];
-      red[((w*6+g+3)<<8) + (i<<6) + l] = t[i];
-    }
-  }
-  __syncthreads();
-  int i = w;
-  int b = b0 + ((l>>4)<<2) + i;
-  int j = j0 + (l&15);
-  float GI[3], GH[3];
-  #pragma unroll
-  for (int pg = 0; pg < 3; ++pg){
-    float a = 0.f, c = 0.f;
-    #pragma unroll
-    for (int ww = 0; ww < 4; ++ww){
-      a += red[((ww*6+pg)<<8)+(i<<6)+l];
-      c += red[((ww*6+pg+3)<<8)+(i<<6)+l];
-    }
-    GI[pg] = a; GH[pg] = c;
-  }
-  float hpv = h2p[(size_t)b*512 + j];
-  float r = sigm(GI[0] + b2ih[j] + GH[0] + b2hh[j]);
-  float zz = sigm(GI[1] + b2ih[512+j] + GH[1] + b2hh[512+j]);
-  float nn = tanhf(GI[2] + b2ih[1024+j] + r*(GH[2] + b2hh[1024+j]));
-  float h = (1.f-zz)*nn + zz*hpv;
-  h2n[(size_t)b*512 + j] = h;
-  unsigned short s0,s1,s2; split3(h,s0,s1,s2);
-  int off = b*512 + j;
-  h2sn[off] = s0; h2sn[off+65536] = s1; h2sn[off+131072] = s2;
-  hsm[(b-b0)*16 + (j-j0)] = h;
-  __syncthreads();
-  if (tid < 144){
-    int bq = tid/9, d = tid - bq*9;
-    float v = 0.f;
-    #pragma unroll
-    for (int jl = 0; jl < 16; ++jl) v += hsm[bq*16+jl]*nfw[(size_t)d*512 + j0 + jl];
-    atomicAdd(&logc[(b0+bq)*9 + d], v);
+    float lg = nfb[d];
+    const float* pl = plog + 36864 + b*9 + d;
+    #pragma unroll
+    for (int q = 0; q < 32; ++q) lg += pl[q*1152];
+    dout[OUT_NR + (size_t)b*2304 + 255*9 + d] = lg;
   }
 }
 
@@ -861,11 +898,6 @@
       dec[((size_t)b*256 + op)*256 + oc] = v;
     }
   }
-}
-
-__global__ void copylast_kern(const float* __restrict__ logit1, float* __restrict__ dout){
-  int idx = blockIdx.x*256 + threadIdx.x;
-  if (idx < 1152) dout[OUT_NR + (size_t)(idx/9)*2304 + 255*9 + (idx % 9)] = logit1[idx];
 }
 
 extern "C" void kernel_launch(void* const* d_in, const int* in_sizes, int n_in,
@@ -946,8 +978,9 @@
   esq_kern<<<dim3(8), dim3(256), 0, stream>>>(embed, ws);
   split_w_kern<<<dim3(1024), dim3(256), 0, stream>>>(gfwhh, gbwhh, ws);
 
-  for (int s = 0; s < 256; ++s){
-    enc_step_mfma<<<dim3(256), dim3(256), 0, stream>>>(ws, note, gfbhh, gbbhh, s);
+  {
+    void* eargs[] = { (void*)&ws, (void*)&note, (void*)&gfbhh, (void*)&gbbhh };
+    hipLaunchCooperativeKernel(enc_persist, dim3(256), dim3(256), eargs, 0, stream);
   }
 
   conv1_kern<<<dim3(256, 8), dim3(256), 0, stream>>>(ysp, ws + O_WT1, c1b, bnsp, ws + O_C1);
@@ -965,10 +998,10 @@
   convt2_kern<<<dim3(512, 4), dim3(256), 0, stream>>>(ws + O_D1, ws + O_WTD2, ct2b, bnsp, ws + O_DEC);
   split_dec_kern<<<dim3(2048), dim3(256), 0, stream>>>(ws);
 
-  for (int i = 0; i < 256; ++i){
-    dec_k1_mfma<<<dim3(256), dim3(256), 0, stream>>>(ws, skel, sr, g1wih, g1bih,
-        g1bhh, nfb, out, i);
-    dec_k2_mfma<<<dim3(256), dim3(256), 0, stream>>>(ws, g2bih, g2bhh, nfw, i);
-  }
-  copylast_kern<<<dim3(5), dim3(256), 0, stream>>>(ws + O_LOG + 1152, out);
-}
+  {
+    void* dargs[] = { (void*)&ws, (void*)&skel, (void*)&sr, (void*)&g1wih,
+                      (void*)&g1bih, (void*)&g1bhh, (void*)&nfb,
+                      (void*)&g2bih, (void*)&g2bhh, (void*)&nfw, (void*)&out };
+    hipLaunchCooperativeKernel(dec_persist, dim3(256), dim3(256), dargs, 0, stream);
+  }
+}
```

After: 28.58 ms. 1.91x slower.
